# Kernel optimization log

Hardware: AMD Instinct MI355X
Metric: run time of the kernel (lower is better)

## Reference

```python
import jax, jax.numpy as jnp
import numpy as np

K = 5
NEG = -1e9
EPS = 1e-5


def _to_pix(f):
    # [B,C,H,W] -> [C,B,H,W] -> [C, B*H*W] -> [B*H*W, C]
    C = f.shape[1]
    return jnp.transpose(f, (1, 0, 2, 3)).reshape(C, -1).T


def _bn(x, g, b):
    # BatchNorm1d in training mode: biased batch statistics
    m = jnp.mean(x, axis=0)
    v = jnp.var(x, axis=0)
    return (x - m) * jax.lax.rsqrt(v + EPS) * g + b


def _transf(x, W1, b1, g1, be1, W2, b2, g2, be2):
    h = jax.nn.relu(_bn(x @ W1.T + b1, g1, be1))
    return jax.nn.relu(_bn(h @ W2.T + b2, g2, be2))


def reference(inp_cont, inp_style, peers_cont, peers_style,
              W1, b1, g1, be1, W2, b2, g2, be2, cw1, cb1, cw2, cb2):
    B, Cs, H, W_ = inp_style.shape
    xi = _to_pix(inp_cont)     # [N, C]
    xp = _to_pix(peers_cont)   # [M, C]
    sp = _to_pix(peers_style)  # [M, Cs]

    # pairwise euclidean distance [N, M]
    d2 = (jnp.sum(xi * xi, axis=1, keepdims=True)
          + jnp.sum(xp * xp, axis=1)[None, :]
          - 2.0 * xi @ xp.T)
    dist = jnp.sqrt(jnp.maximum(d2, 0.0))

    # kth smallest distance per row (top-k of negated distances)
    kth = -jax.lax.top_k(-dist, K)[0][:, K - 1:K]  # [N, 1]

    # additive attention scores: conv1d with kernel_size == feature length == dot product
    ti = _transf(xi, W1, b1, g1, be1, W2, b2, g2, be2)  # [N, C/4]
    tp = _transf(xp, W1, b1, g1, be1, W2, b2, g2, be2)  # [M, C/4]
    a1 = ti @ cw1 + cb1  # [N]
    a2 = tp @ cw2 + cb2  # [M]
    att = a1[:, None] + a2[None, :]  # [N, M]

    knn_filter = jnp.where(dist > kth, NEG, 0.0)
    att = jax.nn.softmax(jax.nn.softplus(att) + knn_filter, axis=1)

    out = att @ sp  # [N, Cs]
    fmap = jnp.transpose(out.T.reshape(Cs, B, H, W_), (1, 0, 2, 3))
    return jnp.concatenate([inp_cont, fmap], axis=1)


def setup_inputs() -> dict:
    key = jax.random.key(0)
    ks = jax.random.split(key, 12)
    C, Cs = 256, 256
    inp = {
        "inp_cont": jax.random.normal(ks[0], (1, C, 64, 64), jnp.float32),
        "inp_style": jax.random.normal(ks[1], (1, Cs, 64, 64), jnp.float32),
        "peers_cont": jax.random.normal(ks[2], (4, C, 64, 64), jnp.float32),
        "peers_style": jax.random.normal(ks[3], (4, Cs, 64, 64), jnp.float32),
        "W1": jax.random.normal(ks[4], (C // 2, C), jnp.float32) * 0.05,
        "b1": jnp.zeros((C // 2,), jnp.float32),
        "g1": jnp.ones((C // 2,), jnp.float32),
        "be1": jnp.zeros((C // 2,), jnp.float32),
        "W2": jax.random.normal(ks[5], (C // 4, C // 2), jnp.float32) * 0.08,
        "b2": jnp.zeros((C // 4,), jnp.float32),
        "g2": jnp.ones((C // 4,), jnp.float32),
        "be2": jnp.zeros((C // 4,), jnp.float32),
        "cw1": jax.random.normal(ks[6], (C // 4,), jnp.float32) * 0.1,
        "cb1": jnp.zeros((), jnp.float32),
        "cw2": jax.random.normal(ks[7], (C // 4,), jnp.float32) * 0.1,
        "cb2": jnp.zeros((), jnp.float32),
    }
    return inp
```

## Files before the change

### kernel.cpp

```cpp
#include <hip/hip_runtime.h>
#include <math.h>

#define NROWS 4096
#define MCOLS 16384
#define CDIM  256

typedef _Float16 half8 __attribute__((ext_vector_type(8)));
typedef float f32x4 __attribute__((ext_vector_type(4)));

static __device__ __forceinline__ float softplusf(float x) {
    return fmaxf(x, 0.0f) + log1pf(expf(-fabsf(x)));
}

#define TOPK_UPDATE(BV, BI, WORST, WP, V, IDX)                                 \
    if ((V) < (WORST)) {                                                       \
        BV[WP] = (V); BI[WP] = (IDX);                                          \
        WORST = BV[0]; WP = 0;                                                 \
        _Pragma("unroll")                                                      \
        for (int _q = 1; _q < 8; ++_q)                                         \
            if (BV[_q] > WORST) { WORST = BV[_q]; WP = _q; }                   \
    }

#define TOPK_FAST(BV, BI, WORST, GATE, TAU, V, IDX)                            \
    if ((V) < (GATE)) {                                                        \
        const int _wp = __float_as_int(WORST) & 7;                             \
        BV[_wp] = __uint_as_float((__float_as_uint(V) & ~7u) | (unsigned)_wp); \
        BI[_wp] = (IDX);                                                       \
        const float _m0 = fmaxf(fmaxf(BV[0], BV[1]), fmaxf(BV[2], BV[3]));     \
        const float _m1 = fmaxf(fmaxf(BV[4], BV[5]), fmaxf(BV[6], BV[7]));     \
        WORST = fmaxf(_m0, _m1);                                               \
        GATE = fminf(TAU, WORST);                                              \
    }

__global__ __launch_bounds__(256)
void copy_kernel(const float4* __restrict__ src, float4* __restrict__ dst, int n4) {
    int i = blockIdx.x * blockDim.x + threadIdx.x;
    if (i < n4) dst[i] = src[i];
}

__global__ __launch_bounds__(256)
void norms_kernel(const float* __restrict__ xiT, const float* __restrict__ xpT,
                  float* __restrict__ normI, float* __restrict__ normP) {
    const int t = threadIdx.x;
    const int col = blockIdx.x * 64 + (t >> 2);
    const int sub = t & 3;
    const float* p;
    int base;
    if (col < MCOLS) { p = xpT; base = (col >> 12) * (CDIM * 4096) + (col & 4095); }
    else             { p = xiT; base = col - MCOLS; }
    float s = 0.0f;
#pragma unroll 8
    for (int k = 0; k < 64; ++k) {
        const float v = p[base + (sub * 64 + k) * 4096];
        s = fmaf(v, v, s);
    }
    s += __shfl_xor(s, 1);
    s += __shfl_xor(s, 2);
    if (sub == 0) {
        if (col < MCOLS) normP[col] = s;
        else             normI[col - MCOLS] = s;
    }
}

__global__ __launch_bounds__(256)
void convert_kernel(const float* __restrict__ src, uint4* __restrict__ dhi,
                    uint4* __restrict__ dlo, int ncols) {
    __shared__ float S[64][65];
    const int t = threadIdx.x;
    const int tilesPerRow = ncols >> 6;
    const int colbase = (blockIdx.x % tilesPerRow) << 6;
    const int ktbase  = (blockIdx.x / tilesPerRow) << 6;
    const int b = colbase >> 12;
    const int pixbase = colbase & 4095;
    const float* sp = src + (size_t)b * (CDIM * 4096) + (size_t)ktbase * 4096 + pixbase;

    for (int i = t; i < 4096; i += 256) {
        int kk = i >> 6, cc = i & 63;
        S[kk][cc] = sp[kk * 4096 + cc];
    }
    __syncthreads();

    const int l = t & 63;
#pragma unroll
    for (int s = 0; s < 2; ++s) {
        const int pid  = (t >> 6) + 4 * s;
        const int ct_l = pid & 3;
        const int kt_l = pid >> 2;
        const int c_l  = ct_l * 16 + (l & 15);
        const int k_l  = kt_l * 32 + ((l >> 4) << 3);
        half8 h, lo;
#pragma unroll
        for (int j = 0; j < 8; ++j) {
            float v = S[k_l + j][c_l];
            _Float16 hv = (_Float16)v;
            h[j]  = hv;
            lo[j] = (_Float16)(v - (float)hv);
        }
        const int ct_g = (colbase >> 4) + ct_l;
        const int kt_g = (ktbase >> 5) + kt_l;
        const size_t off = (size_t)(ct_g * 8 + kt_g) * 64 + l;
        dhi[off] = *reinterpret_cast<uint4*>(&h);
        dlo[off] = *reinterpret_cast<uint4*>(&lo);
    }
}

__global__ __launch_bounds__(256, 2)
void dist_topk_mfma(const uint4* __restrict__ xpBhi, const uint4* __restrict__ xpBlo,
                    const uint4* __restrict__ xiBhi, const uint4* __restrict__ xiBlo,
                    const float* __restrict__ normP,
                    float* __restrict__ candV, int* __restrict__ candI,
                    int nsplit) {
    __shared__ __align__(16) char Abuf[2][32768];
    __shared__ __align__(16) float nPl[2048];

    const int t = threadIdx.x;
    const int w = t >> 6;
    const int l = t & 63;
    int rt, cs;
    if (nsplit == 16) { cs = ((blockIdx.x & 7) << 1) | ((blockIdx.x >> 3) & 1); rt = blockIdx.x >> 4; }
    else              { cs = blockIdx.x & 7;                                    rt = blockIdx.x >> 3; }
    const int niter = (MCOLS / 32) / nsplit;
    const int span  = MCOLS / nsplit;
    const int colbase = cs * span;
    const int ncand = nsplit * 8;

    for (int i = t; i < span; i += 256) nPl[i] = 0.5f * normP[colbase + i];

    uint4 bh[8], bl[8];
    const int ct = rt * 4 + w;
#pragma unroll
    for (int kt = 0; kt < 8; ++kt) {
        bh[kt] = xiBhi[(size_t)(ct * 8 + kt) * 64 + l];
        bl[kt] = xiBlo[(size_t)(ct * 8 + kt) * 64 + l];
    }

    float bv[8]; int bi[8];
#pragma unroll
    for (int j = 0; j < 8; ++j) {
        bv[j] = __uint_as_float((0x7f7ffff8u) | (unsigned)j);
        bi[j] = -1;
    }
    float worst = bv[7], tau = bv[7], gate = bv[7];

    const char* gb = (w >= 2) ? (const char*)xpBlo : (const char*)xpBhi;
    const char* srcBase = gb + (size_t)(cs * niter * 2 + (w & 1)) * 8192 + l * 16;
    char* dbBase = &Abuf[0][(w >> 1) * 16384 + (w & 1) * 8192];

    auto stage = [&](int it, int buf) {
        const char* src = srcBase + (size_t)it * 16384;
        char* db = dbBase + buf * 32768;
#pragma unroll
        for (int kt = 0; kt < 8; ++kt)
            __builtin_amdgcn_global_load_lds(
                (const __attribute__((address_space(1))) void*)(src + kt * 1024),
                (__attribute__((address_space(3))) void*)(db + kt * 1024),
                16, 0, 0);
    };

    stage(0, 0);
    asm volatile("s_waitcnt vmcnt(0)" ::: "memory");
    __builtin_amdgcn_s_barrier();

    for (int it = 0; it < niter; ++it) {
        if (it < niter - 1) {
            stage(it + 1, (it + 1) & 1);
            asm volatile("s_waitcnt vmcnt(8)" ::: "memory");
        } else {
            asm volatile("s_waitcnt vmcnt(0)" ::: "memory");
        }
        __builtin_amdgcn_s_barrier();
        __builtin_amdgcn_sched_barrier(0);

        const char* Ab = Abuf[it & 1];
        const int lo4 = (l >> 4) << 2;

        f32x4 a0[2], a1[2];
#pragma unroll
        for (int c = 0; c < 2; ++c) {
            a0[c] = f32x4{0.f,0.f,0.f,0.f};
            a1[c] = f32x4{0.f,0.f,0.f,0.f};
        }
        __builtin_amdgcn_s_setprio(1);
#pragma unroll
        for (int kt = 0; kt < 8; ++kt) {
            const half8 vh = *reinterpret_cast<const half8*>(&bh[kt]);
            const half8 vl = *reinterpret_cast<const half8*>(&bl[kt]);
#pragma unroll
            for (int c = 0; c < 2; ++c) {
                const half8 ah = *reinterpret_cast<const half8*>(Ab + c * 8192 + kt * 1024 + l * 16);
                const half8 al = *reinterpret_cast<const half8*>(Ab + 16384 + c * 8192 + kt * 1024 + l * 16);
                a0[c] = __builtin_amdgcn_mfma_f32_16x16x32_f16(ah, vh, a0[c], 0, 0, 0);
                a1[c] = __builtin_amdgcn_mfma_f32_16x16x32_f16(ah, vl, a1[c], 0, 0, 0);
                a0[c] = __builtin_amdgcn_mfma_f32_16x16x32_f16(al, vh, a0[c], 0, 0, 0);
            }
        }
        __builtin_amdgcn_s_setprio(0);

        float dv[8];
#pragma unroll
        for (int c = 0; c < 2; ++c) {
            const float4 np4 = *reinterpret_cast<const float4*>(&nPl[it * 32 + c * 16 + lo4]);
            const float npv[4] = {np4.x, np4.y, np4.z, np4.w};
#pragma unroll
            for (int j = 0; j < 4; ++j)
                dv[c * 4 + j] = npv[j] - (a0[c][j] + a1[c][j]);
        }
        const float mn = fminf(fminf(fminf(dv[0], dv[1]), fminf(dv[2], dv[3])),
                               fminf(fminf(dv[4], dv[5]), fminf(dv[6], dv[7])));
        const int ib = colbase + it * 32 + lo4;
        if (__any(mn < gate)) {
#pragma unroll
            for (int q = 0; q < 8; ++q) {
                const int cb = ib + (q >> 2) * 16 + (q & 3);
                TOPK_FAST(bv, bi, worst, gate, tau, dv[q], cb);
            }
        }

        {
            float w1 = fminf(worst, __shfl_xor(worst, 16));
            tau = fminf(w1, __shfl_xor(w1, 32));
            gate = fminf(tau, worst);
        }

        __builtin_amdgcn_s_barrier();
    }

    float* mVal = (float*)&Abuf[0][0];
    int*   mIdx = (int*)&Abuf[0][8192];

    __syncthreads();
#pragma unroll
    for (int j = 0; j < 8; ++j) { mVal[t * 8 + j] = bv[j]; mIdx[t * 8 + j] = bi[j]; }
    __syncthreads();
    if (t < 64) {
        float sv[8]; int si[8];
#pragma unroll
        for (int j = 0; j < 8; ++j) { sv[j] = 3.4e38f; si[j] = -1; }
        float wv = 3.4e38f; int wp = 0;
        for (int g = 0; g < 4; ++g) {
            const int fl = ((t >> 4) << 6) + (t & 15) + 16 * g;
#pragma unroll
            for (int j = 0; j < 8; ++j) {
                const float v = mVal[fl * 8 + j];
                TOPK_UPDATE(sv, si, wv, wp, v, mIdx[fl * 8 + j]);
            }
        }
        for (int a = 1; a < 8; ++a) {
            float v = sv[a]; int ii = si[a]; int b2 = a - 1;
            while (b2 >= 0 && sv[b2] > v) { sv[b2+1] = sv[b2]; si[b2+1] = si[b2]; --b2; }
            sv[b2+1] = v; si[b2+1] = ii;
        }
        const int row = rt * 64 + t;
#pragma unroll
        for (int j = 0; j < 8; ++j) {
            candV[row * ncand + cs * 8 + j] = sv[j];
            candI[row * ncand + cs * 8 + j] = si[j];
        }
    }
}

__global__ __launch_bounds__(256)
void gemm1_kernel(const float* __restrict__ Xp, const float* __restrict__ Xi,
                  const float* __restrict__ W, const float* __restrict__ bias,
                  float* __restrict__ outP, float* __restrict__ outI) {
    __shared__ __align__(16) float Wl[128][68];
    const int t = threadIdx.x;
    const bool isP = blockIdx.x < 512;
    const int bid  = isP ? blockIdx.x : blockIdx.x - 512;
    const float* X = isP ? Xp : Xi;
    const int rows = isP ? 16384 : 4096;
    float* outT = isP ? outP : outI;
    const int rowblk = bid >> 1;
    const int ch     = bid & 1;

    const int r   = rowblk * 64 + (t & 63);
    const int kgb = (t >> 6) * 16;

    float acc[16];
#pragma unroll
    for (int q = 0; q < 16; ++q) acc[q] = 0.0f;

    for (int half = 0; half < 2; ++half) {
        __syncthreads();
        for (int i = t; i < 128 * 64; i += 256) {
            int k = i >> 7, c = i & 127;
            Wl[c][k] = W[(ch * 64 + k) * 256 + half * 128 + c];
        }
        __syncthreads();
#pragma unroll 2
        for (int c = 0; c < 128; ++c) {
            const int cg = half * 128 + c;
            const float x = X[(r >> 12) * (CDIM * 4096) + cg * 4096 + (r & 4095)];
#pragma unroll
            for (int q = 0; q < 4; ++q) {
                const float4 wv = *reinterpret_cast<const float4*>(&Wl[c][kgb + 4 * q]);
                acc[4 * q + 0] = fmaf(x, wv.x, acc[4 * q + 0]);
                acc[4 * q + 1] = fmaf(x, wv.y, acc[4 * q + 1]);
                acc[4 * q + 2] = fmaf(x, wv.z, acc[4 * q + 2]);
                acc[4 * q + 3] = fmaf(x, wv.w, acc[4 * q + 3]);
            }
        }
    }
#pragma unroll
    for (int q = 0; q < 16; ++q) {
        const int k = ch * 64 + kgb + q;
        outT[k * rows + r] = acc[q] + bias[k];
    }
}

__global__ __launch_bounds__(256)
void gemm2_kernel(const float* __restrict__ Hp, const float* __restrict__ Hi,
                  const float* __restrict__ W, const float* __restrict__ bias,
                  const float* __restrict__ statsP, const float* __restrict__ statsI,
                  const float* __restrict__ g, const float* __restrict__ be,
                  float* __restrict__ outP, float* __restrict__ outI) {
    __shared__ __align__(16) float Wl[128][68];
    __shared__ float scL[128], shL[128];
    const int t = threadIdx.x;
    const bool isP = blockIdx.x < 256;
    const float* X = isP ? Hp : Hi;
    const float* stats = isP ? statsP : statsI;
    const float invDenom = isP ? (1.0f / 16384.0f) : (1.0f / 4096.0f);
    const int rows = isP ? 16384 : 4096;
    const int blk  = isP ? blockIdx.x : blockIdx.x - 256;
    float* outT = isP ? outP : outI;

    for (int i = t; i < 128 * 64; i += 256) {
        int k = i >> 7, c = i & 127;
        Wl[c][k] = W[k * 128 + c];
    }
    if (t < 128) {
        float mean = stats[t] * invDenom;
        float var  = stats[128 + t] * invDenom - mean * mean;
        float sc   = rsqrtf(var + 1e-5f) * g[t];
        scL[t] = sc;
        shL[t] = be[t] - mean * sc;
    }
    __syncthreads();

    const int r   = blk * 64 + (t & 63);
    const int chb = (t >> 6) * 16;

    float acc[16];
#pragma unroll
    for (int q = 0; q < 16; ++q) acc[q] = 0.0f;

#pragma unroll 2
    for (int c = 0; c < 128; ++c) {
        float x = X[c * rows + r];
        x = fmaxf(fmaf(x, scL[c], shL[c]), 0.0f);
#pragma unroll
        for (int q = 0; q < 4; ++q) {
            const float4 wv = *reinterpret_cast<const float4*>(&Wl[c][chb + 4 * q]);
            acc[4 * q + 0] = fmaf(x, wv.x, acc[4 * q + 0]);
            acc[4 * q + 1] = fmaf(x, wv.y, acc[4 * q + 1]);
            acc[4 * q + 2] = fmaf(x, wv.z, acc[4 * q + 2]);
            acc[4 * q + 3] = fmaf(x, wv.w, acc[4 * q + 3]);
        }
    }
#pragma unroll
    for (int q = 0; q < 16; ++q) {
        const int k = chb + q;
        outT[k * rows + r] = acc[q] + bias[k];
    }
}

__global__ __launch_bounds__(256)
void colstats2x_kernel(const float* __restrict__ Hp, const float* __restrict__ Hi,
                       int C, float* __restrict__ statsP, float* __restrict__ statsI) {
    __shared__ float rs[256], rq[256];
    const bool isP = blockIdx.x < (unsigned)C;
    const int c = isP ? blockIdx.x : blockIdx.x - C;
    const float* H = isP ? Hp : Hi;
    const int rows = isP ? 16384 : 4096;
    float* stats = isP ? statsP : statsI;
    const int t = threadIdx.x;
    float s = 0.0f, q = 0.0f;
    for (int r = t; r < rows; r += 256) {
        float v = H[c * rows + r];
        s += v;
        q = fmaf(v, v, q);
    }
    rs[t] = s; rq[t] = q;
    __syncthreads();
    for (int st = 128; st > 0; st >>= 1) {
        if (t < st) { rs[t] += rs[t + st]; rq[t] += rq[t + st]; }
        __syncthreads();
    }
    if (t == 0) { stats[c] = rs[0]; stats[C + c] = rq[0]; }
}

__global__ __launch_bounds__(256)
void a2x_kernel(const float* __restrict__ Hp, const float* __restrict__ Hi,
                const float* __restrict__ statsP, const float* __restrict__ statsI,
                const float* __restrict__ g, const float* __restrict__ be,
                const float* __restrict__ cwP, const float* __restrict__ cbP,
                const float* __restrict__ cwI, const float* __restrict__ cbI,
                float* __restrict__ aP, float* __restrict__ aI) {
    __shared__ float scL[64], shL[64], cwL[64];
    const bool isP = blockIdx.x < 64;
    const float* H = isP ? Hp : Hi;
    const float* stats = isP ? statsP : statsI;
    const float* cw = isP ? cwP : cwI;
    const float* cb = isP ? cbP : cbI;
    float* aout = isP ? aP : aI;
    const int rows = isP ? 16384 : 4096;
    const float invDenom = isP ? (1.0f / 16384.0f) : (1.0f / 4096.0f);
    const int blk = isP ? blockIdx.x : blockIdx.x - 64;
    const int t = threadIdx.x;
    if (t < 64) {
        float mean = stats[t] * invDenom;
        float var  = stats[64 + t] * invDenom - mean * mean;
        float sc   = rsqrtf(var + 1e-5f) * g[t];
        scL[t] = sc;
        shL[t] = be[t] - mean * sc;
        cwL[t] = cw[t];
    }
    __syncthreads();
    const int row = blk * 256 + t;
    if (row < rows) {
        float a = 0.0f;
        for (int c = 0; c < 64; ++c) {
            float v = H[c * rows + row];
            a += fmaxf(fmaf(v, scL[c], shL[c]), 0.0f) * cwL[c];
        }
        aout[row] = a + cb[0];
    }
}

__global__ __launch_bounds__(256)
void merge_kernel(const float* __restrict__ candV, const int* __restrict__ candI,
                  const float* __restrict__ a1, const float* __restrict__ a2,
                  float* __restrict__ w8, int* __restrict__ gidx, int ncand) {
    const int row = blockIdx.x * 256 + threadIdx.x;
    float sv[8]; int si[8];
#pragma unroll
    for (int j = 0; j < 8; ++j) { sv[j] = 3.4e38f; si[j] = 0; }
    float w2 = 3.4e38f; int wp = 0;
    for (int k = 0; k < ncand; ++k) {
        const float v = candV[row * ncand + k];
        TOPK_UPDATE(sv, si, w2, wp, v, candI[row * ncand + k]);
    }
    for (int a = 1; a < 8; ++a) {
        float v = sv[a]; int ii = si[a]; int b = a - 1;
        while (b >= 0 && sv[b] > v) { sv[b + 1] = sv[b]; si[b + 1] = si[b]; --b; }
        sv[b + 1] = v; si[b + 1] = ii;
    }
    const float kth = sv[4];
    int cnt = 5;
    while (cnt < 8 && sv[cnt] <= kth) ++cnt;

    const float arow = a1[row];
    float s[8], e[8];
    float mx = -1e30f;
#pragma unroll
    for (int j = 0; j < 8; ++j) s[j] = 0.0f;
    for (int j = 0; j < cnt; ++j) {
        s[j] = softplusf(arow + a2[si[j]]);
        mx = fmaxf(mx, s[j]);
    }
    float Z = 0.0f;
    for (int j = 0; j < 8; ++j) {
        e[j] = (j < cnt) ? expf(s[j] - mx) : 0.0f;
        Z += e[j];
    }
#pragma unroll
    for (int j = 0; j < 8; ++j) {
        const int ix = (j < cnt) ? si[j] : si[0];
        w8[row * 8 + j]   = e[j] / Z;
        gidx[row * 8 + j] = (ix >> 12) * (CDIM * 4096) + (ix & 4095);
    }
}

__global__ __launch_bounds__(256)
void gather_kernel(const float* __restrict__ w8, const int* __restrict__ gidx,
                   const float* __restrict__ PS, float* __restrict__ dout) {
    const int t = threadIdx.x;
    const int rtile = blockIdx.x >> 4;
    const int chunk = blockIdx.x & 15;
    const int row = rtile * 64 + (t & 63);
    const int c0  = chunk * 16 + (t >> 6) * 4;

    float w[8]; int ab[8];
#pragma unroll
    for (int j = 0; j < 8; ++j) { w[j] = w8[row * 8 + j]; ab[j] = gidx[row * 8 + j]; }

#pragma unroll
    for (int cc = 0; cc < 4; ++cc) {
        const int c = c0 + cc;
        float acc = 0.0f;
#pragma unroll
        for (int j = 0; j < 8; ++j) acc += w[j] * PS[ab[j] + c * 4096];
        dout[(CDIM + c) * 4096 + row] = acc;
    }
}

extern "C" void kernel_launch(void* const* d_in, const int* in_sizes, int n_in,
                              void* d_out, int out_size, void* d_ws, size_t ws_size,
                              hipStream_t stream) {
    const float* inp_cont    = (const float*)d_in[0];
    const float* peers_cont  = (const float*)d_in[2];
    const float* peers_style = (const float*)d_in[3];
    const float* W1  = (const float*)d_in[4];
    const float* b1  = (const float*)d_in[5];
    const float* g1  = (const float*)d_in[6];
    const float* be1 = (const float*)d_in[7];
    const float* W2  = (const float*)d_in[8];
    const float* b2  = (const float*)d_in[9];
    const float* g2  = (const float*)d_in[10];
    const float* be2 = (const float*)d_in[11];
    const float* cw1 = (const float*)d_in[12];
    const float* cb1 = (const float*)d_in[13];
    const float* cw2 = (const float*)d_in[14];
    const float* cb2 = (const float*)d_in[15];
    float* out = (float*)d_out;
    char*  wsb = (char*)d_ws;

    int nsplit;
    if      (ws_size >= (size_t)25400000) nsplit = 16;
    else if (ws_size >= (size_t)23300000) nsplit = 8;
    else return;
    const int ncand = nsplit * 8;
    const size_t candBytes = (size_t)NROWS * ncand * 4;

    uint4* xpBhi = (uint4*)(wsb + 0);
    uint4* xpBlo = (uint4*)(wsb + 8388608);
    uint4* xiBhi = (uint4*)(wsb + 16777216);
    uint4* xiBlo = (uint4*)(wsb + 18874368);
    float* normP = (float*)(wsb + 20971520);
    float* normI = (float*)(wsb + 21037056);
    float* candV = (float*)(wsb + 21053440);
    int*   candI = (int*)  (wsb + 21053440 + candBytes);
    char*  tail  = wsb + 21053440 + 2 * candBytes;
    float* a2    = (float*)(tail);
    float* a1    = (float*)(tail + 65536);
    float* s1p   = (float*)(tail + 81920);
    float* s1i   = (float*)(tail + 82944);
    float* s2p   = (float*)(tail + 83968);
    float* s2i   = (float*)(tail + 84480);
    float* H1Tp  = (float*)(wsb + 0);
    float* H2Tp  = (float*)(wsb + 8388608);
    float* H1Ti  = (float*)(wsb + 16777216);
    float* H2Ti  = (float*)(wsb + 18874368);
    float* w8    = (float*)(wsb + 19922944);
    int*   gidx  = (int*)  (wsb + 20054016);

    copy_kernel<<<1024, 256, 0, stream>>>((const float4*)inp_cont, (float4*)out, 262144);
    norms_kernel<<<320, 256, 0, stream>>>(inp_cont, peers_cont, normI, normP);
    convert_kernel<<<256, 256, 0, stream>>>(inp_cont, xiBhi, xiBlo, 4096);
    convert_kernel<<<1024, 256, 0, stream>>>(peers_cont, xpBhi, xpBlo, 16384);

    dist_topk_mfma<<<64 * nsplit, 256, 0, stream>>>(xpBhi, xpBlo, xiBhi, xiBlo,
                                                    normP, candV, candI, nsplit);

    gemm1_kernel<<<640, 256, 0, stream>>>(peers_cont, inp_cont, W1, b1, H1Tp, H1Ti);
    colstats2x_kernel<<<256, 256, 0, stream>>>(H1Tp, H1Ti, 128, s1p, s1i);
    gemm2_kernel<<<320, 256, 0, stream>>>(H1Tp, H1Ti, W2, b2, s1p, s1i, g1, be1, H2Tp, H2Ti);
    colstats2x_kernel<<<128, 256, 0, stream>>>(H2Tp, H2Ti, 64, s2p, s2i);
    a2x_kernel<<<80, 256, 0, stream>>>(H2Tp, H2Ti, s2p, s2i, g2, be2,
                                       cw2, cb2, cw1, cb1, a2, a1);

    merge_kernel<<<16, 256, 0, stream>>>(candV, candI, a1, a2, w8, gidx, ncand);
    gather_kernel<<<1024, 256, 0, stream>>>(w8, gidx, peers_style, out);
}
```

Before: 376.6 us.

## Switch distance kernel to 32x32x16 MFMA tiles with matching operand layout

Changes the fp16 split-precision distance GEMM from 16x16x32 MFMA to 32x32x16 MFMA. The convert kernel's packed layout changes to match, and each wave now covers 32 query rows, so a block covers 128 rows and half as many blocks are launched. Each lane holds twice as many query-operand registers (16 kt steps) and 16 accumulator values per pass, and the per-block top-k merge is reorganised for 128 rows. The aim is more work per LDS load and fewer MFMA issues, at the cost of more register pressure and fewer blocks.

Measured after the change: 343.1 us. 8.9% less time.

```diff
diff --git a/kernel.cpp b/kernel.cpp
--- a/kernel.cpp
+++ b/kernel.cpp
@@ -7,6 +7,7 @@
 
 typedef _Float16 half8 __attribute__((ext_vector_type(8)));
 typedef float f32x4 __attribute__((ext_vector_type(4)));
+typedef float f32x16 __attribute__((ext_vector_type(16)));
 
 static __device__ __forceinline__ float softplusf(float x) {
     return fmaxf(x, 0.0f) + log1pf(expf(-fabsf(x)));
@@ -84,10 +85,10 @@
 #pragma unroll
     for (int s = 0; s < 2; ++s) {
         const int pid  = (t >> 6) + 4 * s;
-        const int ct_l = pid & 3;
-        const int kt_l = pid >> 2;
-        const int c_l  = ct_l * 16 + (l & 15);
-        const int k_l  = kt_l * 32 + ((l >> 4) << 3);
+        const int ct_l = pid & 1;
+        const int kt_l = pid >> 1;
+        const int c_l  = ct_l * 32 + (l & 31);
+        const int k_l  = kt_l * 16 + ((l >> 5) << 3);
         half8 h, lo;
 #pragma unroll
         for (int j = 0; j < 8; ++j) {
@@ -96,9 +97,9 @@
             h[j]  = hv;
             lo[j] = (_Float16)(v - (float)hv);
         }
-        const int ct_g = (colbase >> 4) + ct_l;
-        const int kt_g = (ktbase >> 5) + kt_l;
-        const size_t off = (size_t)(ct_g * 8 + kt_g) * 64 + l;
+        const int ct_g = (colbase >> 5) + ct_l;
+        const int kt_g = (ktbase >> 4) + kt_l;
+        const size_t off = (size_t)(ct_g * 16 + kt_g) * 64 + l;
         dhi[off] = *reinterpret_cast<uint4*>(&h);
         dlo[off] = *reinterpret_cast<uint4*>(&lo);
     }
@@ -126,12 +127,12 @@
 
     for (int i = t; i < span; i += 256) nPl[i] = 0.5f * normP[colbase + i];
 
-    uint4 bh[8], bl[8];
-    const int ct = rt * 4 + w;
-#pragma unroll
-    for (int kt = 0; kt < 8; ++kt) {
-        bh[kt] = xiBhi[(size_t)(ct * 8 + kt) * 64 + l];
-        bl[kt] = xiBlo[(size_t)(ct * 8 + kt) * 64 + l];
+    uint4 bh[16], bl[16];
+    const int ctg = rt * 4 + w;
+#pragma unroll
+    for (int kt = 0; kt < 16; ++kt) {
+        bh[kt] = xiBhi[(size_t)(ctg * 16 + kt) * 64 + l];
+        bl[kt] = xiBlo[(size_t)(ctg * 16 + kt) * 64 + l];
     }
 
     float bv[8]; int bi[8];
@@ -143,8 +144,8 @@
     float worst = bv[7], tau = bv[7], gate = bv[7];
 
     const char* gb = (w >= 2) ? (const char*)xpBlo : (const char*)xpBhi;
-    const char* srcBase = gb + (size_t)(cs * niter * 2 + (w & 1)) * 8192 + l * 16;
-    char* dbBase = &Abuf[0][(w >> 1) * 16384 + (w & 1) * 8192];
+    const char* srcBase = gb + (size_t)(cs * niter) * 16384 + (w & 1) * 8192 + l * 16;
+    char* dbBase = &Abuf[0][(w >= 2 ? 16384 : 0) + (w & 1) * 8192];
 
     auto stage = [&](int it, int buf) {
         const char* src = srcBase + (size_t)it * 16384;
@@ -172,53 +173,49 @@
         __builtin_amdgcn_sched_barrier(0);
 
         const char* Ab = Abuf[it & 1];
-        const int lo4 = (l >> 4) << 2;
-
-        f32x4 a0[2], a1[2];
-#pragma unroll
-        for (int c = 0; c < 2; ++c) {
-            a0[c] = f32x4{0.f,0.f,0.f,0.f};
-            a1[c] = f32x4{0.f,0.f,0.f,0.f};
-        }
+
+        f32x16 a0, a1;
+#pragma unroll
+        for (int r = 0; r < 16; ++r) { a0[r] = 0.0f; a1[r] = 0.0f; }
         __builtin_amdgcn_s_setprio(1);
 #pragma unroll
-        for (int kt = 0; kt < 8; ++kt) {
+        for (int kt = 0; kt < 16; ++kt) {
+            const half8 ah = *reinterpret_cast<const half8*>(Ab + kt * 1024 + l * 16);
+            const half8 al = *reinterpret_cast<const half8*>(Ab + 16384 + kt * 1024 + l * 16);
             const half8 vh = *reinterpret_cast<const half8*>(&bh[kt]);
             const half8 vl = *reinterpret_cast<const half8*>(&bl[kt]);
-#pragma unroll
-            for (int c = 0; c < 2; ++c) {
-                const half8 ah = *reinterpret_cast<const half8*>(Ab + c * 8192 + kt * 1024 + l * 16);
-                const half8 al = *reinterpret_cast<const half8*>(Ab + 16384 + c * 8192 + kt * 1024 + l * 16);
-                a0[c] = __builtin_amdgcn_mfma_f32_16x16x32_f16(ah, vh, a0[c], 0, 0, 0);
-                a1[c] = __builtin_amdgcn_mfma_f32_16x16x32_f16(ah, vl, a1[c], 0, 0, 0);
-                a0[c] = __builtin_amdgcn_mfma_f32_16x16x32_f16(al, vh, a0[c], 0, 0, 0);
+            a0 = __builtin_amdgcn_mfma_f32_32x32x16_f16(ah, vh, a0, 0, 0, 0);
+            a1 = __builtin_amdgcn_mfma_f32_32x32x16_f16(ah, vl, a1, 0, 0, 0);
+            a0 = __builtin_amdgcn_mfma_f32_32x32x16_f16(al, vh, a0, 0, 0, 0);
+        }
+        __builtin_amdgcn_s_setprio(0);
+
+        float dv[16];
+        const int lq = (l >> 5) << 2;
+#pragma unroll
+        for (int rq = 0; rq < 4; ++rq) {
+            const float4 np4 = *reinterpret_cast<const float4*>(&nPl[it * 32 + rq * 8 + lq]);
+            const float npv[4] = {np4.x, np4.y, np4.z, np4.w};
+#pragma unroll
+            for (int j = 0; j < 4; ++j) {
+                const int r = rq * 4 + j;
+                dv[r] = npv[j] - (a0[r] + a1[r]);
             }
         }
-        __builtin_amdgcn_s_setprio(0);
-
-        float dv[8];
-#pragma unroll
-        for (int c = 0; c < 2; ++c) {
-            const float4 np4 = *reinterpret_cast<const float4*>(&nPl[it * 32 + c * 16 + lo4]);
-            const float npv[4] = {np4.x, np4.y, np4.z, np4.w};
-#pragma unroll
-            for (int j = 0; j < 4; ++j)
-                dv[c * 4 + j] = npv[j] - (a0[c][j] + a1[c][j]);
-        }
-        const float mn = fminf(fminf(fminf(dv[0], dv[1]), fminf(dv[2], dv[3])),
-                               fminf(fminf(dv[4], dv[5]), fminf(dv[6], dv[7])));
-        const int ib = colbase + it * 32 + lo4;
+        float mn = dv[0];
+#pragma unroll
+        for (int r = 1; r < 16; ++r) mn = fminf(mn, dv[r]);
+        const int ib = colbase + it * 32 + lq;
         if (__any(mn < gate)) {
 #pragma unroll
-            for (int q = 0; q < 8; ++q) {
-                const int cb = ib + (q >> 2) * 16 + (q & 3);
-                TOPK_FAST(bv, bi, worst, gate, tau, dv[q], cb);
+            for (int r = 0; r < 16; ++r) {
+                const int cb = ib + (r & 3) + 8 * (r >> 2);
+                TOPK_FAST(bv, bi, worst, gate, tau, dv[r], cb);
             }
         }
 
         {
-            float w1 = fminf(worst, __shfl_xor(worst, 16));
-            tau = fminf(w1, __shfl_xor(w1, 32));
+            tau = fminf(worst, __shfl_xor(worst, 32));
             gate = fminf(tau, worst);
         }
 
@@ -232,25 +229,26 @@
 #pragma unroll
     for (int j = 0; j < 8; ++j) { mVal[t * 8 + j] = bv[j]; mIdx[t * 8 + j] = bi[j]; }
     __syncthreads();
-    if (t < 64) {
+    if (t < 128) {
+        const int t1 = ((t >> 5) << 6) + (t & 31);
+        const int t2 = t1 + 32;
         float sv[8]; int si[8];
 #pragma unroll
         for (int j = 0; j < 8; ++j) { sv[j] = 3.4e38f; si[j] = -1; }
         float wv = 3.4e38f; int wp = 0;
-        for (int g = 0; g < 4; ++g) {
-            const int fl = ((t >> 4) << 6) + (t & 15) + 16 * g;
-#pragma unroll
-            for (int j = 0; j < 8; ++j) {
-                const float v = mVal[fl * 8 + j];
-                TOPK_UPDATE(sv, si, wv, wp, v, mIdx[fl * 8 + j]);
-            }
+#pragma unroll
+        for (int j = 0; j < 8; ++j) {
+            const float v1 = mVal[t1 * 8 + j];
+            TOPK_UPDATE(sv, si, wv, wp, v1, mIdx[t1 * 8 + j]);
+            const float v2 = mVal[t2 * 8 + j];
+            TOPK_UPDATE(sv, si, wv, wp, v2, mIdx[t2 * 8 + j]);
         }
         for (int a = 1; a < 8; ++a) {
             float v = sv[a]; int ii = si[a]; int b2 = a - 1;
             while (b2 >= 0 && sv[b2] > v) { sv[b2+1] = sv[b2]; si[b2+1] = si[b2]; --b2; }
             sv[b2+1] = v; si[b2+1] = ii;
         }
-        const int row = rt * 64 + t;
+        const int row = rt * 128 + t;
 #pragma unroll
         for (int j = 0; j < 8; ++j) {
             candV[row * ncand + cs * 8 + j] = sv[j];
@@ -550,7 +548,7 @@
     convert_kernel<<<256, 256, 0, stream>>>(inp_cont, xiBhi, xiBlo, 4096);
     convert_kernel<<<1024, 256, 0, stream>>>(peers_cont, xpBhi, xpBlo, 16384);
 
-    dist_topk_mfma<<<64 * nsplit, 256, 0, stream>>>(xpBhi, xpBlo, xiBhi, xiBlo,
+    dist_topk_mfma<<<32 * nsplit, 256, 0, stream>>>(xpBhi, xpBlo, xiBhi, xiBlo,
                                                     normP, candV, candI, nsplit);
 
     gemm1_kernel<<<640, 256, 0, stream>>>(peers_cont, inp_cont, W1, b1, H1Tp, H1Ti);
```
